# Performance work log

Measured on AMD Instinct MI355X. Metric: run time of the kernel, lower is better.

The kernel has to match this reference:

```python
import jax, jax.numpy as jnp
import numpy as np
from math import atanh

B, T, D_IN, H = 16, 1024, 512, 1024
INIT_A = atanh(0.95)


def setup_inputs() -> dict:
    key = jax.random.key(0)
    k1, k2, k3, k4 = jax.random.split(key, 4)
    x = jax.random.normal(k1, (B, T, D_IN), dtype=jnp.float32)
    h0 = jax.random.normal(k2, (B, H), dtype=jnp.float32)
    # raw_a initialized near atanh(0.95) as in the module, with small jitter
    raw_a = INIT_A + 0.01 * jax.random.normal(k3, (H,), dtype=jnp.float32)
    # xavier-uniform for W_x.weight [H, D_IN]
    limit = float(np.sqrt(6.0 / (D_IN + H)))
    W = jax.random.uniform(k4, (H, D_IN), dtype=jnp.float32, minval=-limit, maxval=limit)
    b = jnp.zeros((H,), dtype=jnp.float32)
    return {"x": x, "h0": h0, "raw_a": raw_a, "W": W, "b": b}


def reference(x, h0, raw_a, W, b):
    # h_t = a * h_{t-1} + W x_t + b, computed via cumprod/cumsum parallel-scan trick
    a = jnp.tanh(raw_a)                                   # [H] (rho is None)
    z = jnp.einsum('btd,hd->bth', x, W) + b               # [B,T,H]
    A = jnp.broadcast_to(a, (x.shape[1], a.shape[0]))     # [T,H]
    p = jnp.cumprod(A, axis=0)[None]                      # [1,T,H], p[t] = a^(t+1)
    v = jnp.cumsum(z / jnp.maximum(p, 1e-12), axis=1)     # [B,T,H]
    h = v * p + p * h0[:, None, :]                        # include initial state
    zero_mask = (jnp.abs(a) < 1e-6)[None, None, :]        # degenerate a ~ 0 channels
    h = jnp.where(zero_mask, z, h)
    return h
```

## Files before the change

kernel.cpp:

```cpp
#include <hip/hip_runtime.h>
#include <cstdint>

#define B_DIM 16
#define T_DIM 1024
#define DK    512
#define H_DIM 1024

typedef __bf16 bf16x8 __attribute__((ext_vector_type(8)));
typedef __bf16 bf16x4 __attribute__((ext_vector_type(4)));
typedef float  f32x4  __attribute__((ext_vector_type(4)));

typedef __attribute__((address_space(1))) unsigned int* as1p;
typedef __attribute__((address_space(3))) unsigned int* as3p;

__device__ __forceinline__ void async_cp16(const void* g, void* l) {
  __builtin_amdgcn_global_load_lds((as1p)(uint64_t)g,
                                   (as3p)(uint32_t)(uint64_t)l, 16, 0, 0);
}

__global__ __launch_bounds__(256) void cvt_f32_bf16(const float* __restrict__ in,
                                                    __bf16* __restrict__ out, int n4) {
  int i = blockIdx.x * 256 + threadIdx.x;
  if (i >= n4) return;
  f32x4 v = ((const f32x4*)in)[i];
  bf16x4 o;
  o.x = (__bf16)v.x; o.y = (__bf16)v.y; o.z = (__bf16)v.z; o.w = (__bf16)v.w;
  ((bf16x4*)out)[i] = o;
}

__global__ __launch_bounds__(256) void compute_meta(const float* __restrict__ raw_a,
                                                    float4* __restrict__ meta) {
  int h = blockIdx.x * 256 + threadIdx.x;
  if (h >= H_DIM) return;
  float a = tanhf(raw_a[h]);
  float la2 = log2f(fabsf(a));
  meta[h] = make_float4(a, la2, (a < 0.f) ? 1.f : 0.f, (fabsf(a) < 1e-6f) ? 1.f : 0.f);
}

__global__ __launch_bounds__(256, 2) void fused_rnn(const __bf16* __restrict__ xb,
                                                    const __bf16* __restrict__ wb,
                                                    const float* __restrict__ bias,
                                                    const float4* __restrict__ meta,
                                                    const float* __restrict__ h0g,
                                                    float* __restrict__ out) {
  __shared__ __align__(16) __bf16 As[256 * 32];
  __shared__ __align__(16) __bf16 Bs[32 * 32];
  __shared__ float chunkTot[4][32];
  __shared__ float colCarry[32];

  const int tid  = threadIdx.x;
  const int wave = tid >> 6;
  const int lane = tid & 63;
  const int q = lane >> 4;
  const int c = lane & 15;

  const int b    = blockIdx.x & 15;
  const int n0   = (blockIdx.x >> 4) * 32;

  float bias_j[2], la2_j[2], h0_j[2];
  bool neg_j[2], zm_j[2];
#pragma unroll
  for (int j = 0; j < 2; ++j) {
    const int col = n0 + j * 16 + c;
    bias_j[j] = bias[col];
    const float4 mt = meta[col];
    la2_j[j] = mt.y;
    neg_j[j] = mt.z != 0.f;
    zm_j[j]  = mt.w != 0.f;
    h0_j[j]  = h0g[(size_t)b * H_DIM + col];
  }

  if (tid < 32) colCarry[tid] = 0.f;

  const int srow = lane >> 2;
  const int skof = (lane & 3) * 8;

  for (int mc = 0; mc < 4; ++mc) {
    const int t0 = mc * 256;
    const __bf16* Abase = xb + (size_t)(b * T_DIM + t0) * DK;

    f32x4 acc[4][2];
#pragma unroll
    for (int i = 0; i < 4; ++i)
#pragma unroll
      for (int j = 0; j < 2; ++j) acc[i][j] = (f32x4){0.f, 0.f, 0.f, 0.f};

    for (int k0 = 0; k0 < DK; k0 += 32) {
      __syncthreads();
#pragma unroll
      for (int r = 0; r < 4; ++r) {
        const int s = wave * 4 + r;
        const __bf16* ga = Abase + (size_t)(s * 16 + srow) * DK + k0 + skof;
        async_cp16(ga, As + s * 16 * 32);
      }
      if (wave < 2) {
        const __bf16* gb = wb + (size_t)(n0 + wave * 16 + srow) * DK + k0 + skof;
        async_cp16(gb, Bs + wave * 16 * 32);
      }
      __syncthreads();
      bf16x8 af[4], bfr[2];
#pragma unroll
      for (int i = 0; i < 4; ++i)
        af[i] = *(const bf16x8*)(As + (wave * 64 + i * 16 + c) * 32 + q * 8);
#pragma unroll
      for (int j = 0; j < 2; ++j)
        bfr[j] = *(const bf16x8*)(Bs + (j * 16 + c) * 32 + q * 8);
#pragma unroll
      for (int i = 0; i < 4; ++i)
#pragma unroll
        for (int j = 0; j < 2; ++j)
          acc[i][j] = __builtin_amdgcn_mfma_f32_16x16x32_bf16(af[i], bfr[j], acc[i][j], 0, 0, 0);
    }

    f32x4 vloc[4][2];
    float icarry[2] = {0.f, 0.f};
#pragma unroll
    for (int i = 0; i < 4; ++i) {
#pragma unroll
      for (int j = 0; j < 2; ++j) {
        const float la2 = la2_j[j];
        f32x4 w;
#pragma unroll
        for (int r = 0; r < 4; ++r) {
          const int tp1 = t0 + wave * 64 + i * 16 + q * 4 + r + 1;
          const float z = acc[i][j][r] + bias_j[j];
          float inv = fminf(__builtin_amdgcn_exp2f(-la2 * (float)tp1), 1e12f);
          if (neg_j[j] && (tp1 & 1)) inv = 1e12f;
          w[r] = z * inv;
        }
        const float pr0 = w[0];
        const float pr1 = pr0 + w[1];
        const float pr2 = pr1 + w[2];
        const float pr3 = pr2 + w[3];
        const float x1 = __shfl_xor(pr3, 16, 64);
        const float x2 = __shfl_xor(pr3, 32, 64);
        const float x3 = __shfl_xor(pr3, 48, 64);
        float sq = 0.f;
        if (q >= 2) sq += x2 + x3;
        if (q & 1) sq += x1;
        const float base = icarry[j] + sq;
        vloc[i][j] = (f32x4){base + pr0, base + pr1, base + pr2, base + pr3};
        icarry[j] += pr3 + x1 + x2 + x3;
      }
    }
    if (q == 0) {
#pragma unroll
      for (int j = 0; j < 2; ++j) chunkTot[wave][j * 16 + c] = icarry[j];
    }
    __syncthreads();

    float cc[2];
#pragma unroll
    for (int j = 0; j < 2; ++j) {
      float s = colCarry[j * 16 + c];
      for (int w2 = 0; w2 < 4; ++w2)
        if (w2 < wave) s += chunkTot[w2][j * 16 + c];
      cc[j] = s;
    }
#pragma unroll
    for (int i = 0; i < 4; ++i) {
#pragma unroll
      for (int j = 0; j < 2; ++j) {
        const float la2 = la2_j[j];
        const int col = n0 + j * 16 + c;
#pragma unroll
        for (int r = 0; r < 4; ++r) {
          const int tl = t0 + wave * 64 + i * 16 + q * 4 + r;
          const int tp1 = tl + 1;
          float pv = __builtin_amdgcn_exp2f(la2 * (float)tp1);
          if (neg_j[j] && (tp1 & 1)) pv = -pv;
          const float v = cc[j] + vloc[i][j][r];
          const float hv = pv * v + pv * h0_j[j];
          const float zval = acc[i][j][r] + bias_j[j];
          out[(size_t)(b * T_DIM + tl) * H_DIM + col] = zm_j[j] ? zval : hv;
        }
      }
    }
    __syncthreads();
    if (tid < 32)
      colCarry[tid] += chunkTot[0][tid] + chunkTot[1][tid] + chunkTot[2][tid] + chunkTot[3][tid];
  }
}

extern "C" void kernel_launch(void* const* d_in, const int* in_sizes, int n_in,
                              void* d_out, int out_size, void* d_ws, size_t ws_size,
                              hipStream_t stream) {
  const float* x     = (const float*)d_in[0];
  const float* h0    = (const float*)d_in[1];
  const float* raw_a = (const float*)d_in[2];
  const float* W     = (const float*)d_in[3];
  const float* bias  = (const float*)d_in[4];
  float* out = (float*)d_out;

  char* ws = (char*)d_ws;
  __bf16* xb   = (__bf16*)(ws);
  __bf16* wb   = (__bf16*)(ws + 16777216);
  float4* meta = (float4*)(ws + 16777216 + 1048576);

  cvt_f32_bf16<<<(B_DIM * T_DIM * DK / 4 + 255) / 256, 256, 0, stream>>>(x, xb, B_DIM * T_DIM * DK / 4);
  cvt_f32_bf16<<<(H_DIM * DK / 4 + 255) / 256, 256, 0, stream>>>(W, wb, H_DIM * DK / 4);
  compute_meta<<<H_DIM / 256, 256, 0, stream>>>(raw_a, meta);
  fused_rnn<<<512, 256, 0, stream>>>(xb, wb, bias, meta, h0, out);
}
```

Before: 146.7 us.

## Double-buffer LDS tiles with K=64 steps and prefetch across M chunks

Replaces the single-buffer load/sync/compute GEMM loop with a double-buffered pipeline. The next K tile, and the first tile of the next time chunk, is issued via async global-to-LDS copies while MFMAs run on the current buffer. Each step now covers 64 K elements, which halves the number of barriers per chunk. LDS use per block roughly quadruples, which may reduce occupancy. Correctness depends on the async copies having landed before the single barrier at the end of each step.

```diff
diff --git a/kernel.cpp b/kernel.cpp
--- a/kernel.cpp
+++ b/kernel.cpp
@@ -43,8 +43,8 @@
                                                     const float4* __restrict__ meta,
                                                     const float* __restrict__ h0g,
                                                     float* __restrict__ out) {
-  __shared__ __align__(16) __bf16 As[256 * 32];
-  __shared__ __align__(16) __bf16 Bs[32 * 32];
+  __shared__ __align__(16) __bf16 As[2][2][256][32];
+  __shared__ __align__(16) __bf16 Bs[2][2][32][32];
   __shared__ float chunkTot[4][32];
   __shared__ float colCarry[32];
 
@@ -54,8 +54,8 @@
   const int q = lane >> 4;
   const int c = lane & 15;
 
-  const int b    = blockIdx.x & 15;
-  const int n0   = (blockIdx.x >> 4) * 32;
+  const int b  = blockIdx.x & 15;
+  const int n0 = (blockIdx.x >> 4) * 32;
 
   float bias_j[2], la2_j[2], h0_j[2];
   bool neg_j[2], zm_j[2];
@@ -75,9 +75,30 @@
   const int srow = lane >> 2;
   const int skof = (lane & 3) * 8;
 
+  const __bf16* const xbB = xb + (size_t)b * T_DIM * DK;
+
+  auto stage = [&](int t0, int k0, int buf) {
+#pragma unroll
+    for (int h = 0; h < 2; ++h) {
+#pragma unroll
+      for (int r = 0; r < 4; ++r) {
+        const int rg = wave * 64 + r * 16;
+        const __bf16* ga = xbB + (size_t)(t0 + rg + srow) * DK + k0 + h * 32 + skof;
+        async_cp16(ga, &As[buf][h][rg][0]);
+      }
+    }
+    {
+      const int h = wave >> 1, rp = (wave & 1) * 16;
+      const __bf16* gb = wb + (size_t)(n0 + rp + srow) * DK + k0 + (wave >> 1) * 32 + skof;
+      async_cp16(gb, &Bs[buf][h][rp][0]);
+    }
+  };
+
+  stage(0, 0, 0);
+  __syncthreads();
+
   for (int mc = 0; mc < 4; ++mc) {
     const int t0 = mc * 256;
-    const __bf16* Abase = xb + (size_t)(b * T_DIM + t0) * DK;
 
     f32x4 acc[4][2];
 #pragma unroll
@@ -85,31 +106,26 @@
 #pragma unroll
       for (int j = 0; j < 2; ++j) acc[i][j] = (f32x4){0.f, 0.f, 0.f, 0.f};
 
-    for (int k0 = 0; k0 < DK; k0 += 32) {
+    for (int k = 0; k < 8; ++k) {
+      const int buf = k & 1;
+      if (k < 7)       stage(t0, (k + 1) * 64, buf ^ 1);
+      else if (mc < 3) stage(t0 + 256, 0, 0);
+#pragma unroll
+      for (int ks = 0; ks < 2; ++ks) {
+        bf16x8 af[4], bfr[2];
+#pragma unroll
+        for (int i = 0; i < 4; ++i)
+          af[i] = *(const bf16x8*)(&As[buf][ks][wave * 64 + i * 16 + c][q * 8]);
+#pragma unroll
+        for (int j = 0; j < 2; ++j)
+          bfr[j] = *(const bf16x8*)(&Bs[buf][ks][j * 16 + c][q * 8]);
+#pragma unroll
+        for (int i = 0; i < 4; ++i)
+#pragma unroll
+          for (int j = 0; j < 2; ++j)
+            acc[i][j] = __builtin_amdgcn_mfma_f32_16x16x32_bf16(af[i], bfr[j], acc[i][j], 0, 0, 0);
+      }
       __syncthreads();
-#pragma unroll
-      for (int r = 0; r < 4; ++r) {
-        const int s = wave * 4 + r;
-        const __bf16* ga = Abase + (size_t)(s * 16 + srow) * DK + k0 + skof;
-        async_cp16(ga, As + s * 16 * 32);
-      }
-      if (wave < 2) {
-        const __bf16* gb = wb + (size_t)(n0 + wave * 16 + srow) * DK + k0 + skof;
-        async_cp16(gb, Bs + wave * 16 * 32);
-      }
-      __syncthreads();
-      bf16x8 af[4], bfr[2];
-#pragma unroll
-      for (int i = 0; i < 4; ++i)
-        af[i] = *(const bf16x8*)(As + (wave * 64 + i * 16 + c) * 32 + q * 8);
-#pragma unroll
-      for (int j = 0; j < 2; ++j)
-        bfr[j] = *(const bf16x8*)(Bs + (j * 16 + c) * 32 + q * 8);
-#pragma unroll
-      for (int i = 0; i < 4; ++i)
-#pragma unroll
-        for (int j = 0; j < 2; ++j)
-          acc[i][j] = __builtin_amdgcn_mfma_f32_16x16x32_bf16(af[i], bfr[j], acc[i][j], 0, 0, 0);
     }
 
     f32x4 vloc[4][2];
```

After: 137.7 us. 1.07x faster.

## Preload full W tile into LDS, read x directly to registers, use 8 waves

Applied to the files above, without the earlier changes.

The fused RNN kernel now loads the block's entire 32xK weight slice into padded LDS once, and each wave reads its x rows from global memory straight into MFMA operand registers. The per-k double-barrier async staging of A tiles into LDS goes away. Block size doubles to 512 threads with 32 time rows per wave, and the column carry is double-buffered to drop one barrier per chunk. The intent is to remove the per-k-step synchronization and LDS traffic. In exchange, x is read from global memory without LDS staging, which may lose coalescing and makes the kernel rely on cache and latency hiding.

```diff
diff --git a/kernel.cpp b/kernel.cpp
--- a/kernel.cpp
+++ b/kernel.cpp
@@ -5,18 +5,11 @@
 #define T_DIM 1024
 #define DK    512
 #define H_DIM 1024
+#define BST   516
 
 typedef __bf16 bf16x8 __attribute__((ext_vector_type(8)));
 typedef __bf16 bf16x4 __attribute__((ext_vector_type(4)));
 typedef float  f32x4  __attribute__((ext_vector_type(4)));
-
-typedef __attribute__((address_space(1))) unsigned int* as1p;
-typedef __attribute__((address_space(3))) unsigned int* as3p;
-
-__device__ __forceinline__ void async_cp16(const void* g, void* l) {
-  __builtin_amdgcn_global_load_lds((as1p)(uint64_t)g,
-                                   (as3p)(uint32_t)(uint64_t)l, 16, 0, 0);
-}
 
 __global__ __launch_bounds__(256) void cvt_f32_bf16(const float* __restrict__ in,
                                                     __bf16* __restrict__ out, int n4) {
@@ -37,16 +30,15 @@
   meta[h] = make_float4(a, la2, (a < 0.f) ? 1.f : 0.f, (fabsf(a) < 1e-6f) ? 1.f : 0.f);
 }
 
-__global__ __launch_bounds__(256, 2) void fused_rnn(const __bf16* __restrict__ xb,
+__global__ __launch_bounds__(512, 4) void fused_rnn(const __bf16* __restrict__ xb,
                                                     const __bf16* __restrict__ wb,
                                                     const float* __restrict__ bias,
                                                     const float4* __restrict__ meta,
                                                     const float* __restrict__ h0g,
                                                     float* __restrict__ out) {
-  __shared__ __align__(16) __bf16 As[256 * 32];
-  __shared__ __align__(16) __bf16 Bs[32 * 32];
-  __shared__ float chunkTot[4][32];
-  __shared__ float colCarry[32];
+  __shared__ __align__(16) __bf16 Bs[32][BST];
+  __shared__ float chunkTot[8][32];
+  __shared__ float colCarry[2][32];
 
   const int tid  = threadIdx.x;
   const int wave = tid >> 6;
@@ -54,8 +46,8 @@
   const int q = lane >> 4;
   const int c = lane & 15;
 
-  const int b    = blockIdx.x & 15;
-  const int n0   = (blockIdx.x >> 4) * 32;
+  const int b  = blockIdx.x & 15;
+  const int n0 = (blockIdx.x >> 4) * 32;
 
   float bias_j[2], la2_j[2], h0_j[2];
   bool neg_j[2], zm_j[2];
@@ -70,59 +62,53 @@
     h0_j[j]  = h0g[(size_t)b * H_DIM + col];
   }
 
-  if (tid < 32) colCarry[tid] = 0.f;
+  {
+    const int col = tid >> 4;
+    const int kc  = tid & 15;
+    const __bf16* gw = wb + (size_t)(n0 + col) * DK + kc * 32;
+#pragma unroll
+    for (int u = 0; u < 4; ++u)
+      *(bf16x8*)&Bs[col][kc * 32 + u * 8] = *(const bf16x8*)(gw + u * 8);
+  }
+  if (tid < 32) colCarry[0][tid] = 0.f;
+  __syncthreads();
 
-  const int srow = lane >> 2;
-  const int skof = (lane & 3) * 8;
+  const __bf16* const xbB = xb + (size_t)b * T_DIM * DK;
 
   for (int mc = 0; mc < 4; ++mc) {
     const int t0 = mc * 256;
-    const __bf16* Abase = xb + (size_t)(b * T_DIM + t0) * DK;
 
-    f32x4 acc[4][2];
+    f32x4 acc[2][2];
 #pragma unroll
-    for (int i = 0; i < 4; ++i)
+    for (int i = 0; i < 2; ++i)
 #pragma unroll
       for (int j = 0; j < 2; ++j) acc[i][j] = (f32x4){0.f, 0.f, 0.f, 0.f};
 
-    for (int k0 = 0; k0 < DK; k0 += 32) {
-      __syncthreads();
+    const __bf16* const Arow0 = xbB + (size_t)(t0 + wave * 32 + c) * DK + q * 8;
+    const __bf16* const Arow1 = Arow0 + (size_t)16 * DK;
 #pragma unroll
-      for (int r = 0; r < 4; ++r) {
-        const int s = wave * 4 + r;
-        const __bf16* ga = Abase + (size_t)(s * 16 + srow) * DK + k0 + skof;
-        async_cp16(ga, As + s * 16 * 32);
-      }
-      if (wave < 2) {
-        const __bf16* gb = wb + (size_t)(n0 + wave * 16 + srow) * DK + k0 + skof;
-        async_cp16(gb, Bs + wave * 16 * 32);
-      }
-      __syncthreads();
-      bf16x8 af[4], bfr[2];
-#pragma unroll
-      for (int i = 0; i < 4; ++i)
-        af[i] = *(const bf16x8*)(As + (wave * 64 + i * 16 + c) * 32 + q * 8);
-#pragma unroll
-      for (int j = 0; j < 2; ++j)
-        bfr[j] = *(const bf16x8*)(Bs + (j * 16 + c) * 32 + q * 8);
-#pragma unroll
-      for (int i = 0; i < 4; ++i)
-#pragma unroll
-        for (int j = 0; j < 2; ++j)
-          acc[i][j] = __builtin_amdgcn_mfma_f32_16x16x32_bf16(af[i], bfr[j], acc[i][j], 0, 0, 0);
+    for (int k = 0; k < 16; ++k) {
+      const bf16x8 af0 = *(const bf16x8*)(Arow0 + k * 32);
+      const bf16x8 af1 = *(const bf16x8*)(Arow1 + k * 32);
+      const bf16x8 bf0 = *(const bf16x8*)&Bs[c][k * 32 + q * 8];
+      const bf16x8 bf1 = *(const bf16x8*)&Bs[16 + c][k * 32 + q * 8];
+      acc[0][0] = __builtin_amdgcn_mfma_f32_16x16x32_bf16(af0, bf0, acc[0][0], 0, 0, 0);
+      acc[0][1] = __builtin_amdgcn_mfma_f32_16x16x32_bf16(af0, bf1, acc[0][1], 0, 0, 0);
+      acc[1][0] = __builtin_amdgcn_mfma_f32_16x16x32_bf16(af1, bf0, acc[1][0], 0, 0, 0);
+      acc[1][1] = __builtin_amdgcn_mfma_f32_16x16x32_bf16(af1, bf1, acc[1][1], 0, 0, 0);
     }
 
-    f32x4 vloc[4][2];
+    f32x4 vloc[2][2];
     float icarry[2] = {0.f, 0.f};
 #pragma unroll
-    for (int i = 0; i < 4; ++i) {
+    for (int i = 0; i < 2; ++i) {
 #pragma unroll
       for (int j = 0; j < 2; ++j) {
         const float la2 = la2_j[j];
         f32x4 w;
 #pragma unroll
         for (int r = 0; r < 4; ++r) {
-          const int tp1 = t0 + wave * 64 + i * 16 + q * 4 + r + 1;
+          const int tp1 = t0 + wave * 32 + i * 16 + q * 4 + r + 1;
           const float z = acc[i][j][r] + bias_j[j];
           float inv = fminf(__builtin_amdgcn_exp2f(-la2 * (float)tp1), 1e12f);
           if (neg_j[j] && (tp1 & 1)) inv = 1e12f;
@@ -152,20 +138,26 @@
     float cc[2];
 #pragma unroll
     for (int j = 0; j < 2; ++j) {
-      float s = colCarry[j * 16 + c];
-      for (int w2 = 0; w2 < 4; ++w2)
-        if (w2 < wave) s += chunkTot[w2][j * 16 + c];
+      float s = colCarry[mc & 1][j * 16 + c];
+      for (int w2 = 0; w2 < wave; ++w2) s += chunkTot[w2][j * 16 + c];
       cc[j] = s;
     }
+    if (tid < 32) {
+      float s = colCarry[mc & 1][tid];
 #pragma unroll
-    for (int i = 0; i < 4; ++i) {
+      for (int w2 = 0; w2 < 8; ++w2) s += chunkTot[w2][tid];
+      colCarry[(mc + 1) & 1][tid] = s;
+    }
+
+#pragma unroll
+    for (int i = 0; i < 2; ++i) {
 #pragma unroll
       for (int j = 0; j < 2; ++j) {
         const float la2 = la2_j[j];
         const int col = n0 + j * 16 + c;
 #pragma unroll
         for (int r = 0; r < 4; ++r) {
-          const int tl = t0 + wave * 64 + i * 16 + q * 4 + r;
+          const int tl = t0 + wave * 32 + i * 16 + q * 4 + r;
           const int tp1 = tl + 1;
           float pv = __builtin_amdgcn_exp2f(la2 * (float)tp1);
           if (neg_j[j] && (tp1 & 1)) pv = -pv;
@@ -177,8 +169,6 @@
       }
     }
     __syncthreads();
-    if (tid < 32)
-      colCarry[tid] += chunkTot[0][tid] + chunkTot[1][tid] + chunkTot[2][tid] + chunkTot[3][tid];
   }
 }
 
@@ -200,5 +190,5 @@
   cvt_f32_bf16<<<(B_DIM * T_DIM * DK / 4 + 255) / 256, 256, 0, stream>>>(x, xb, B_DIM * T_DIM * DK / 4);
   cvt_f32_bf16<<<(H_DIM * DK / 4 + 255) / 256, 256, 0, stream>>>(W, wb, H_DIM * DK / 4);
   compute_meta<<<H_DIM / 256, 256, 0, stream>>>(raw_a, meta);
-  fused_rnn<<<512, 256, 0, stream>>>(xb, wb, bias, meta, h0, out);
+  fused_rnn<<<512, 512, 0, stream>>>(xb, wb, bias, meta, h0, out);
 }
```

Measured after the change: 162.6 us. +10.8%, slower.
